# Optimization experiments

Measured on AMD Instinct MI355X. Metric: run time of the kernel, lower is better.

Reference implementation:

```python
import jax, jax.numpy as jnp
import numpy as np

B, T, D_MODEL = 1, 2048, 4096
NUM_Q_HEADS, NUM_KV_HEADS, KEY_SIZE = 32, 8, 128
ATTN_MULT = 0.08838834764831845  # 1/sqrt(key_size)
MAX_ATTN_VAL = 30.0


def rotate_half(x):
    x1, x2 = jnp.split(x, 2, axis=-1)
    return jnp.concatenate((-x2, x1), axis=-1)


def apply_rope(x):
    # x: [b, t, h, d]; offset = 0, positions = arange(t)
    b, t, h, d = x.shape
    exponents = jnp.arange(0, d, 2, dtype=jnp.float32)
    inv_freq = 1.0 / (10000.0 ** (exponents / d))            # [d/2]
    pos = jnp.arange(t, dtype=jnp.float32)                   # [t]
    phase = pos[:, None] * inv_freq[None, :]                 # [t, d/2]
    phase = jnp.tile(phase, (1, 2))[None, :, None, :]        # [1, t, 1, d] (tiled, not interleaved)
    return (x * jnp.cos(phase) + rotate_half(x) * jnp.sin(phase)).astype(x.dtype)


def setup_inputs() -> dict:
    key = jax.random.key(0)
    ks = jax.random.split(key, 8)
    query = jax.random.normal(ks[0], (B, T, D_MODEL), dtype=jnp.float32)
    kk = jax.random.normal(ks[1], (B, T, D_MODEL), dtype=jnp.float32)
    vv = jax.random.normal(ks[2], (B, T, D_MODEL), dtype=jnp.float32)
    mask = jnp.tril(jnp.ones((T, T), dtype=bool))[None, None, :, :]  # causal [1,1,T,T]
    s = 0.02
    Wq = jax.random.normal(ks[3], (D_MODEL, NUM_Q_HEADS * KEY_SIZE), dtype=jnp.float32) * s
    Wk = jax.random.normal(ks[4], (D_MODEL, NUM_KV_HEADS * KEY_SIZE), dtype=jnp.float32) * s
    Wv = jax.random.normal(ks[5], (D_MODEL, NUM_KV_HEADS * KEY_SIZE), dtype=jnp.float32) * s
    Wo = jax.random.normal(ks[6], (NUM_Q_HEADS * KEY_SIZE, D_MODEL), dtype=jnp.float32) * s
    return {"query": query, "key": kk, "value": vv, "mask": mask,
            "Wq": Wq, "Wk": Wk, "Wv": Wv, "Wo": Wo}


def reference(query, key, value, mask, Wq, Wk, Wv, Wo):
    b, t, _ = query.shape
    d = KEY_SIZE
    h, kv_h = NUM_Q_HEADS, NUM_KV_HEADS
    g = h // kv_h
    # projections (no bias)
    q = (query @ Wq).reshape(b, t, h, d)
    k = (key @ Wk).reshape(b, t, kv_h, d)
    v = (value @ Wv).reshape(b, t, kv_h, d)
    # RoPE on q and k
    q = apply_rope(q)
    k = apply_rope(k)
    # GQA grouping: [b, t, kv_h, g, d]
    q = q.reshape(b, t, kv_h, g, d)
    logits = jnp.einsum('btkgd,bTkd->bkgtT', q, k).astype(jnp.float32)
    logits = logits * ATTN_MULT
    logits = MAX_ATTN_VAL * jnp.tanh(logits / MAX_ATTN_VAL)  # soft-capping
    m = mask[:, :, None, :, :]  # [b,1,1,t,T]
    logits = jnp.where(m, logits, -1e30)
    weights = jax.nn.softmax(logits, axis=-1).astype(query.dtype)
    attn = jnp.einsum('bkgtT,bTkd->btkgd', weights, v)
    attn = attn.reshape(b, t, h * d)
    return attn @ Wo
```

## Files before the change

### kernel.cpp

```cpp
#include <hip/hip_runtime.h>
#include <hip/hip_bf16.h>
#include <stdint.h>
#include <stddef.h>

#define T_SEQ 2048
#define DM    4096
#define NQH   32
#define NKVH  8
#define HD    128
#define ATTN_MULT 0.08838834764831845f

typedef __attribute__((ext_vector_type(8))) short bf16x8;
typedef __attribute__((ext_vector_type(4))) float f32x4;
typedef __attribute__((ext_vector_type(4))) unsigned int u32x4;

__device__ __forceinline__ unsigned short f2b(float f) {
  unsigned u = __builtin_bit_cast(unsigned, f);
  u = u + 0x7FFFu + ((u >> 16) & 1u);
  return (unsigned short)(u >> 16);
}
__device__ __forceinline__ float b2f(unsigned short h) {
  unsigned u = ((unsigned)h) << 16;
  return __builtin_bit_cast(float, u);
}

typedef const __attribute__((address_space(1))) void* gptr1_t;
typedef __attribute__((address_space(3))) void* lptr3_t;
__device__ __forceinline__ void gl_lds16(const void* g, void* l) {
  __builtin_amdgcn_global_load_lds((gptr1_t)g, (lptr3_t)l, 16, 0, 0);
}

#define MFMA16(a, b, c) __builtin_amdgcn_mfma_f32_16x16x32_bf16((a), (b), (c), 0, 0, 0)

__global__ __launch_bounds__(256) void transpose_cast4_kernel(
    const float* __restrict__ Wq, const float* __restrict__ Wk,
    const float* __restrict__ Wv, const float* __restrict__ Wo,
    unsigned short* __restrict__ WqT, unsigned short* __restrict__ WkT,
    unsigned short* __restrict__ WvT, unsigned short* __restrict__ WoT) {
  __shared__ float tile[64][65];
  int y = blockIdx.y;
  const float* W;
  unsigned short* WT;
  int N, n0;
  if (y < 64)      { W = Wq; WT = WqT; N = 4096; n0 = y * 64; }
  else if (y < 80) { W = Wk; WT = WkT; N = 1024; n0 = (y - 64) * 64; }
  else if (y < 96) { W = Wv; WT = WvT; N = 1024; n0 = (y - 80) * 64; }
  else             { W = Wo; WT = WoT; N = 4096; n0 = (y - 96) * 64; }
  const int K = 4096;
  int k0 = blockIdx.x * 64;
  int t = threadIdx.x;
  int rr = t >> 4;
  int cc = t & 15;
#pragma unroll
  for (int c = 0; c < 4; ++c) {
    int row = c * 16 + rr;
    float4 v = *(const float4*)&W[(size_t)(k0 + row) * N + n0 + cc * 4];
    tile[row][cc * 4 + 0] = v.x;
    tile[row][cc * 4 + 1] = v.y;
    tile[row][cc * 4 + 2] = v.z;
    tile[row][cc * 4 + 3] = v.w;
  }
  __syncthreads();
  int orow = t >> 2;
  int kb = (t & 3) * 16;
  u32x4 o1, o2;
#pragma unroll
  for (int u = 0; u < 4; ++u) {
    o1[u] = (unsigned)f2b(tile[kb + 2 * u][orow]) |
            ((unsigned)f2b(tile[kb + 2 * u + 1][orow]) << 16);
    o2[u] = (unsigned)f2b(tile[kb + 8 + 2 * u][orow]) |
            ((unsigned)f2b(tile[kb + 9 + 2 * u][orow]) << 16);
  }
  unsigned short* dst = &WT[(size_t)(n0 + orow) * K + k0 + kb];
  *(u32x4*)dst = o1;
  *(u32x4*)(dst + 8) = o2;
}

__global__ __launch_bounds__(256) void cast3_kernel(
    const float* __restrict__ a0, const float* __restrict__ a1, const float* __restrict__ a2,
    unsigned short* __restrict__ b0, unsigned short* __restrict__ b1, unsigned short* __restrict__ b2) {
  const float* in = blockIdx.z == 0 ? a0 : (blockIdx.z == 1 ? a1 : a2);
  unsigned short* out = blockIdx.z == 0 ? b0 : (blockIdx.z == 1 ? b1 : b2);
  size_t idx = ((size_t)blockIdx.x * 256 + threadIdx.x) * 8;
  float4 x = *(const float4*)(in + idx);
  float4 y = *(const float4*)(in + idx + 4);
  u32x4 v;
  v[0] = (unsigned)f2b(x.x) | ((unsigned)f2b(x.y) << 16);
  v[1] = (unsigned)f2b(x.z) | ((unsigned)f2b(x.w) << 16);
  v[2] = (unsigned)f2b(y.x) | ((unsigned)f2b(y.y) << 16);
  v[3] = (unsigned)f2b(y.z) | ((unsigned)f2b(y.w) << 16);
  *(u32x4*)(out + idx) = v;
}

template <bool F32OUT>
__device__ __forceinline__ void gemm_dp_body(
    unsigned short* lds,
    const unsigned short* __restrict__ A, const unsigned short* __restrict__ BT,
    void* __restrict__ C, int N, int K, int m0, int n0) {
  int t = threadIdx.x;
  int w = t >> 6, l = t & 63;
  int wm = w >> 2, wn = w & 3;
  int lr = l & 15, lh = l >> 4;

  f32x4 acc[4][4] = {};

  int lrow8 = l >> 3;
  int scb = ((l & 7) ^ lrow8) << 4;
  const int NT = K >> 6;

  auto stage2 = [&](int tt, int bsel, int c0) {
    int kb = tt * 64;
#pragma unroll
    for (int c = 0; c < 2; ++c) {
      int chunk = w * 6 + c0 + c;
      if (chunk < 16) {
        const char* src = (const char*)A +
            ((size_t)(m0 + chunk * 8 + lrow8) * K + kb) * 2 + scb;
        gl_lds16(src, (char*)lds + bsel * 49152 + chunk * 1024);
      } else {
        const char* src = (const char*)BT +
            ((size_t)(n0 + (chunk - 16) * 8 + lrow8) * K + kb) * 2 + scb;
        gl_lds16(src, (char*)lds + bsel * 49152 + 16384 + (chunk - 16) * 1024);
      }
    }
  };

  stage2(0, 0, 0); stage2(0, 0, 2); stage2(0, 0, 4);
  stage2(1, 1, 0); stage2(1, 1, 2); stage2(1, 1, 4);
  asm volatile("s_waitcnt vmcnt(6)" ::: "memory");
  __builtin_amdgcn_s_barrier();

  int bsel = 0, bnext = 2;
  for (int tt = 0; tt < NT; ++tt) {
    bool pre = (tt + 2 < NT);
    const char* Ab = (const char*)lds + bsel * 49152;
    const char* Bb = Ab + 16384;
    int rswz = (lr & 7) << 4;
    int arow = wm * 64 + lr;
    int brow = wn * 64 + lr;
    int cb0 = (lh * 16) ^ rswz;
    int cb1 = (64 + lh * 16) ^ rswz;

    bf16x8 a0 = *(const bf16x8*)(Ab + (arow + 0) * 128 + cb0);
    bf16x8 a1 = *(const bf16x8*)(Ab + (arow + 16) * 128 + cb0);
    bf16x8 b0 = *(const bf16x8*)(Bb + (brow + 0) * 128 + cb0);
    bf16x8 b1 = *(const bf16x8*)(Bb + (brow + 16) * 128 + cb0);
    bf16x8 b2 = *(const bf16x8*)(Bb + (brow + 32) * 128 + cb0);
    bf16x8 b3 = *(const bf16x8*)(Bb + (brow + 48) * 128 + cb0);
    if (pre) stage2(tt + 2, bnext, 0);
    __builtin_amdgcn_s_barrier();
    __builtin_amdgcn_s_setprio(1);
    acc[0][0] = MFMA16(a0, b0, acc[0][0]);
    acc[0][1] = MFMA16(a0, b1, acc[0][1]);
    acc[0][2] = MFMA16(a0, b2, acc[0][2]);
    acc[0][3] = MFMA16(a0, b3, acc[0][3]);
    acc[1][0] = MFMA16(a1, b0, acc[1][0]);
    acc[1][1] = MFMA16(a1, b1, acc[1][1]);
    acc[1][2] = MFMA16(a1, b2, acc[1][2]);
    acc[1][3] = MFMA16(a1, b3, acc[1][3]);
    __builtin_amdgcn_s_setprio(0);
    __builtin_amdgcn_s_barrier();

    a0 = *(const bf16x8*)(Ab + (arow + 32) * 128 + cb0);
    a1 = *(const bf16x8*)(Ab + (arow + 48) * 128 + cb0);
    if (pre) stage2(tt + 2, bnext, 2);
    __builtin_amdgcn_s_barrier();
    __builtin_amdgcn_s_setprio(1);
    acc[2][0] = MFMA16(a0, b0, acc[2][0]);
    acc[2][1] = MFMA16(a0, b1, acc[2][1]);
    acc[2][2] = MFMA16(a0, b2, acc[2][2]);
    acc[2][3] = MFMA16(a0, b3, acc[2][3]);
    acc[3][0] = MFMA16(a1, b0, acc[3][0]);
    acc[3][1] = MFMA16(a1, b1, acc[3][1]);
    acc[3][2] = MFMA16(a1, b2, acc[3][2]);
    acc[3][3] = MFMA16(a1, b3, acc[3][3]);
    __builtin_amdgcn_s_setprio(0);
    __builtin_amdgcn_s_barrier();

    a0 = *(const bf16x8*)(Ab + (arow + 0) * 128 + cb1);
    a1 = *(const bf16x8*)(Ab + (arow + 16) * 128 + cb1);
    b0 = *(const bf16x8*)(Bb + (brow + 0) * 128 + cb1);
    b1 = *(const bf16x8*)(Bb + (brow + 16) * 128 + cb1);
    b2 = *(const bf16x8*)(Bb + (brow + 32) * 128 + cb1);
    b3 = *(const bf16x8*)(Bb + (brow + 48) * 128 + cb1);
    if (pre) stage2(tt + 2, bnext, 4);
    __builtin_amdgcn_s_barrier();
    __builtin_amdgcn_s_setprio(1);
    acc[0][0] = MFMA16(a0, b0, acc[0][0]);
    acc[0][1] = MFMA16(a0, b1, acc[0][1]);
    acc[0][2] = MFMA16(a0, b2, acc[0][2]);
    acc[0][3] = MFMA16(a0, b3, acc[0][3]);
    acc[1][0] = MFMA16(a1, b0, acc[1][0]);
    acc[1][1] = MFMA16(a1, b1, acc[1][1]);
    acc[1][2] = MFMA16(a1, b2, acc[1][2]);
    acc[1][3] = MFMA16(a1, b3, acc[1][3]);
    __builtin_amdgcn_s_setprio(0);
    __builtin_amdgcn_s_barrier();

    a0 = *(const bf16x8*)(Ab + (arow + 32) * 128 + cb1);
    a1 = *(const bf16x8*)(Ab + (arow + 48) * 128 + cb1);
    __builtin_amdgcn_s_barrier();
    __builtin_amdgcn_s_setprio(1);
    acc[2][0] = MFMA16(a0, b0, acc[2][0]);
    acc[2][1] = MFMA16(a0, b1, acc[2][1]);
    acc[2][2] = MFMA16(a0, b2, acc[2][2]);
    acc[2][3] = MFMA16(a0, b3, acc[2][3]);
    acc[3][0] = MFMA16(a1, b0, acc[3][0]);
    acc[3][1] = MFMA16(a1, b1, acc[3][1]);
    acc[3][2] = MFMA16(a1, b2, acc[3][2]);
    acc[3][3] = MFMA16(a1, b3, acc[3][3]);
    __builtin_amdgcn_s_setprio(0);
    if (pre) asm volatile("s_waitcnt vmcnt(6)" ::: "memory");
    else     asm volatile("s_waitcnt vmcnt(0)" ::: "memory");
    __builtin_amdgcn_s_barrier();
    bsel = (bsel == 2) ? 0 : bsel + 1;
    bnext = (bnext == 2) ? 0 : bnext + 1;
  }

#pragma unroll
  for (int i = 0; i < 4; ++i) {
#pragma unroll
    for (int j = 0; j < 4; ++j) {
#pragma unroll
      for (int r = 0; r < 4; ++r) {
        int row = m0 + wm * 64 + i * 16 + lh * 4 + r;
        int col = n0 + wn * 64 + j * 16 + lr;
        if constexpr (F32OUT)
          ((float*)C)[(size_t)row * N + col] = acc[i][j][r];
        else
          ((unsigned short*)C)[(size_t)row * N + col] = f2b(acc[i][j][r]);
      }
    }
  }
}

__global__ __launch_bounds__(512, 1) void qkv_dp_kernel(
    const unsigned short* __restrict__ qb, const unsigned short* __restrict__ WqT, unsigned short* __restrict__ Qp,
    const unsigned short* __restrict__ kb, const unsigned short* __restrict__ WkT, unsigned short* __restrict__ Kp,
    const unsigned short* __restrict__ vb, const unsigned short* __restrict__ WvT, unsigned short* __restrict__ Vp) {
  __shared__ unsigned short lds[3 * 24576];
  int flat = blockIdx.x;
  const unsigned short *A, *BT;
  unsigned short* C;
  int N, m0, n0;
  if (flat < 256) {
    A = qb; BT = WqT; C = Qp; N = NQH * HD;
    int xcd = flat & 7, idx = flat >> 3;
    n0 = (xcd * 2 + (idx & 1)) * 256;
    m0 = (idx >> 1) * 128;
  } else {
    int lf = flat - 256;
    int sel = lf >> 6;
    int local = lf & 63;
    A = sel ? vb : kb;
    BT = sel ? WvT : WkT;
    C = sel ? Vp : Kp;
    N = NKVH * HD;
    m0 = (local >> 2) * 128;
    n0 = (local & 3) * 256;
  }
  gemm_dp_body<false>(lds, A, BT, C, N, DM, m0, n0);
}

__global__ __launch_bounds__(512, 1) void gemm_dp_kernel(
    const unsigned short* __restrict__ A, const unsigned short* __restrict__ BT,
    float* __restrict__ C, int M, int N, int K) {
  __shared__ unsigned short lds[3 * 24576];
  int nx = gridDim.x;
  int flat = blockIdx.y * nx + blockIdx.x;
  int npx = nx >> 3;
  int xcd = flat & 7, idx = flat >> 3;
  int n0 = (xcd * npx + idx % npx) * 256;
  int m0 = (idx / npx) * 128;
  gemm_dp_body<true>(lds, A, BT, C, N, K, m0, n0);
}

__global__ __launch_bounds__(256) void sincos_kernel(float2* __restrict__ tab) {
  int idx = blockIdx.x * 256 + threadIdx.x;
  int i = idx & 63;
  int tpos = idx >> 6;
  float invf = exp2f(-(float)i * (13.287712379549449f / 64.0f));
  float phase = (float)tpos * invf;
  float s, c;
  sincosf(phase, &s, &c);
  tab[idx] = make_float2(c, s);
}

__global__ __launch_bounds__(256) void rope_kernel(unsigned short* __restrict__ X,
                                                   const float2* __restrict__ tab,
                                                   int hshift, float scale) {
  int idx = blockIdx.x * 256 + threadIdx.x;
  int i = idx & 63;
  int rest = idx >> 6;
  int nheads = 1 << hshift;
  int hh = rest & (nheads - 1);
  int tpos = rest >> hshift;
  float2 cs = tab[tpos * 64 + i];
  size_t base = (size_t)tpos * ((size_t)nheads * HD) + (size_t)hh * HD + i;
  float x1 = b2f(X[base]);
  float x2 = b2f(X[base + 64]);
  X[base] = f2b((x1 * cs.x - x2 * cs.y) * scale);
  X[base + 64] = f2b((x2 * cs.x + x1 * cs.y) * scale);
}

__global__ __launch_bounds__(256) void vtrans_kernel(
    const unsigned short* __restrict__ V, unsigned short* __restrict__ VT) {
  size_t flat = ((size_t)blockIdx.x * 256 + threadIdx.x) * 8;
  int t8 = (int)(flat & (T_SEQ - 1));
  int dh = (int)(flat >> 11);
  u32x4 v;
#pragma unroll
  for (int u = 0; u < 4; ++u) {
    unsigned short lo = V[(size_t)(t8 + 2 * u) * (NKVH * HD) + dh];
    unsigned short hi = V[(size_t)(t8 + 2 * u + 1) * (NKVH * HD) + dh];
    v[u] = (unsigned)lo | ((unsigned)hi << 16);
  }
  *(u32x4*)(VT + flat) = v;
}

template <bool DIAG>
__device__ __forceinline__ void softmax_frag(const f32x4 s[4], float& lsum, bf16x8 pf[2],
                                             int lr, int lh, int wq) {
  constexpr float C2f = (float)(-60.0 * 1.4426950408889634);
  float pv[4][4];
#pragma unroll
  for (int ct = 0; ct < 4; ++ct)
#pragma unroll
    for (int r = 0; r < 4; ++r) {
      float u = exp2f(s[ct][r]);
      float p = exp2f(C2f * __builtin_amdgcn_rcpf(u + 1.0f));
      if constexpr (DIAG) {
        int kg = ct * 16 + lh * 4 + r;
        int qg = wq * 16 + lr;
        if (kg > qg) p = 0.0f;
      }
      pv[ct][r] = p;
      lsum += p;
    }
  unsigned pk[4][2];
#pragma unroll
  for (int ct = 0; ct < 4; ++ct) {
    pk[ct][0] = (unsigned)f2b(pv[ct][0]) | ((unsigned)f2b(pv[ct][1]) << 16);
    pk[ct][1] = (unsigned)f2b(pv[ct][2]) | ((unsigned)f2b(pv[ct][3]) << 16);
  }
  int s0 = ((lh & 1) << 5) + lr;
  int s1 = s0 + 16;
  bool hi = (lh >= 2);
#pragma unroll
  for (int ks = 0; ks < 2; ++ks) {
    unsigned a0 = (unsigned)__shfl((int)pk[2 * ks][0], s0, 64);
    unsigned a1 = (unsigned)__shfl((int)pk[2 * ks][1], s0, 64);
    unsigned a2 = (unsigned)__shfl((int)pk[2 * ks][0], s1, 64);
    unsigned a3 = (unsigned)__shfl((int)pk[2 * ks][1], s1, 64);
    unsigned b0 = (unsigned)__shfl((int)pk[2 * ks + 1][0], s0, 64);
    unsigned b1 = (unsigned)__shfl((int)pk[2 * ks + 1][1], s0, 64);
    unsigned b2 = (unsigned)__shfl((int)pk[2 * ks + 1][0], s1, 64);
    unsigned b3 = (unsigned)__shfl((int)pk[2 * ks + 1][1], s1, 64);
    u32x4 f;
    f[0] = hi ? b0 : a0;
    f[1] = hi ? b1 : a1;
    f[2] = hi ? b2 : a2;
    f[3] = hi ? b3 : a3;
    pf[ks] = __builtin_bit_cast(bf16x8, f);
  }
}

template <bool WITHA, bool DIAGA, bool DIAGB>
__device__ __forceinline__ void attn_tile(
    const char* KsCur, const char* VsCur,
    const bf16x8 qfA[4], const bf16x8 qfB[4],
    f32x4 oaccA[8], f32x4 oaccB[8],
    float& lsumA, float& lsumB,
    int lr, int lh, int wq) {
  f32x4 sB[4], sA[4];
#pragma unroll
  for (int ct = 0; ct < 4; ++ct) {
    f32x4 zB = {};
    f32x4 zA = {};
#pragma unroll
    for (int kk = 0; kk < 4; ++kk) {
      int row = ct * 16 + lr;
      int cb = (kk * 32 + lh * 8) * 2;
      bf16x8 kf = *(const bf16x8*)(KsCur + row * 256 + (cb ^ ((row & 7) << 4)));
      zB = MFMA16(kf, qfB[kk], zB);
      if constexpr (WITHA) zA = MFMA16(kf, qfA[kk], zA);
    }
    sB[ct] = zB;
    if constexpr (WITHA) sA[ct] = zA;
  }
  bf16x8 pfB[2], pfA[2];
  softmax_frag<DIAGB>(sB, lsumB, pfB, lr, lh, wq);
  if constexpr (WITHA) softmax_frag<DIAGA>(sA, lsumA, pfA, lr, lh, wq);
#pragma unroll
  for (int ks = 0; ks < 2; ++ks) {
    int pcb = (ks * 32 + lh * 8) * 2;
#pragma unroll
    for (int dt = 0; dt < 8; ++dt) {
      int vrow = dt * 16 + lr;
      bf16x8 vf = *(const bf16x8*)(VsCur + ((vrow * 128 + pcb) ^ ((vrow & 7) << 4)));
      oaccB[dt] = MFMA16(pfB[ks], vf, oaccB[dt]);
      if constexpr (WITHA) oaccA[dt] = MFMA16(pfA[ks], vf, oaccA[dt]);
    }
  }
}

__global__ __launch_bounds__(512, 2) void attn_kernel(
    const unsigned short* __restrict__ Q,
    const unsigned short* __restrict__ Kx,
    const unsigned short* __restrict__ VT,
    unsigned short* __restrict__ O) {
  __shared__ unsigned short Ks[2][64 * 128];
  __shared__ unsigned short Vs[2][128 * 64];

  int bx = blockIdx.x;
  int by = blockIdx.y;
  int qtA = bx, qtB = 31 - bx;
  int t = threadIdx.x;
  int w = t >> 6, l = t & 63;
  int wq = w & 3;
  int hh = by * 2 + (w >> 2);
  int kvh = by >> 1;
  int lr = l & 15, lh = l >> 4;

  bf16x8 qfA[4], qfB[4];
  {
    const unsigned short* qpA = Q + (size_t)(qtA * 64 + wq * 16 + lr) * (NQH * HD) + hh * HD + lh * 8;
    const unsigned short* qpB = Q + (size_t)(qtB * 64 + wq * 16 + lr) * (NQH * HD) + hh * HD + lh * 8;
#pragma unroll
    for (int kk = 0; kk < 4; ++kk) {
      qfA[kk] = *(const bf16x8*)(qpA + kk * 32);
      qfB[kk] = *(const bf16x8*)(qpB + kk * 32);
    }
  }

  f32x4 oaccA[8] = {}, oaccB[8] = {};
  float lsumA = 0.f, lsumB = 0.f;

  const char* KgB = (const char*)Kx + (size_t)kvh * HD * 2;
  const char* VgB = (const char*)VT + (size_t)kvh * HD * T_SEQ * 2;

  auto stage = [&](int kt, int b) {
#pragma unroll
    for (int c = 0; c < 2; ++c) {
      int chunk = w * 2 + c;
      int p = chunk * 1024 + l * 16;
      {
        int row = p >> 8;
        int cb = p & 255;
        int cbl = cb ^ ((row & 7) << 4);
        gl_lds16(KgB + (size_t)(kt * 64 + row) * (NKVH * HD * 2) + cbl,
                 (char*)Ks[b] + chunk * 1024);
      }
      {
        int row = p >> 7;
        int cb = p & 127;
        int cbl = cb ^ ((row & 7) << 4);
        gl_lds16(VgB + (size_t)row * (T_SEQ * 2) + (size_t)kt * 128 + cbl,
                 (char*)Vs[b] + chunk * 1024);
      }
    }
  };

  stage(0, 0);
  __syncthreads();

  int cur = 0;
  for (int kt = 0; kt <= qtB; ++kt) {
    if (kt < qtB) stage(kt + 1, cur ^ 1);
    const char* Kc = (const char*)Ks[cur];
    const char* Vc = (const char*)Vs[cur];
    if (kt < qtA)
      attn_tile<true, false, false>(Kc, Vc, qfA, qfB, oaccA, oaccB, lsumA, lsumB, lr, lh, wq);
    else if (kt == qtA)
      attn_tile<true, true, false>(Kc, Vc, qfA, qfB, oaccA, oaccB, lsumA, lsumB, lr, lh, wq);
    else if (kt < qtB)
      attn_tile<false, false, false>(Kc, Vc, qfA, qfB, oaccA, oaccB, lsumA, lsumB, lr, lh, wq);
    else
      attn_tile<false, false, true>(Kc, Vc, qfA, qfB, oaccA, oaccB, lsumA, lsumB, lr, lh, wq);
    __syncthreads();
    cur ^= 1;
  }

  lsumB += __shfl_xor(lsumB, 16, 64);
  lsumB += __shfl_xor(lsumB, 32, 64);
  lsumA += __shfl_xor(lsumA, 16, 64);
  lsumA += __shfl_xor(lsumA, 32, 64);

#pragma unroll
  for (int i = 0; i < 4; ++i) {
    int srcl = (l & 48) | (lh * 4 + i);
    float invB = 1.0f / __shfl(lsumB, srcl, 64);
    float invA = 1.0f / __shfl(lsumA, srcl, 64);
    int qgB = qtB * 64 + wq * 16 + lh * 4 + i;
    int qgA = qtA * 64 + wq * 16 + lh * 4 + i;
#pragma unroll
    for (int dt = 0; dt < 8; ++dt) {
      O[(size_t)qgB * (NQH * HD) + hh * HD + dt * 16 + lr] = f2b(oaccB[dt][i] * invB);
      O[(size_t)qgA * (NQH * HD) + hh * HD + dt * 16 + lr] = f2b(oaccA[dt][i] * invA);
    }
  }
}

extern "C" void kernel_launch(void* const* d_in, const int* in_sizes, int n_in,
                              void* d_out, int out_size, void* d_ws, size_t ws_size,
                              hipStream_t stream) {
  const float* query = (const float*)d_in[0];
  const float* key = (const float*)d_in[1];
  const float* value = (const float*)d_in[2];
  const float* Wq = (const float*)d_in[4];
  const float* Wk = (const float*)d_in[5];
  const float* Wv = (const float*)d_in[6];
  const float* Wo = (const float*)d_in[7];
  float* out = (float*)d_out;

  char* ws = (char*)d_ws;
  constexpr size_t OFF_WQT = 0;
  constexpr size_t OFF_WOT = 33554432;
  constexpr size_t OFF_WKT = 67108864;
  constexpr size_t OFF_WVT = 75497472;
  constexpr size_t OFF_QB = 83886080;
  constexpr size_t OFF_KB = 100663296;
  constexpr size_t OFF_VB = 117440512;
  constexpr size_t OFF_QP = 134217728;
  constexpr size_t OFF_KP = 150994944;
  constexpr size_t OFF_VP = 155189248;
  constexpr size_t OFF_VT = 159383552;
  constexpr size_t OFF_AT = 163577856;
  constexpr size_t WS_NEED = 180355072;
  if (ws_size < WS_NEED) return;

  unsigned short* WqT = (unsigned short*)(ws + OFF_WQT);
  unsigned short* WoT = (unsigned short*)(ws + OFF_WOT);
  unsigned short* WkT = (unsigned short*)(ws + OFF_WKT);
  unsigned short* WvT = (unsigned short*)(ws + OFF_WVT);
  unsigned short* qb = (unsigned short*)(ws + OFF_QB);
  unsigned short* kb = (unsigned short*)(ws + OFF_KB);
  unsigned short* vb = (unsigned short*)(ws + OFF_VB);
  unsigned short* Qp = (unsigned short*)(ws + OFF_QP);
  unsigned short* Kp = (unsigned short*)(ws + OFF_KP);
  unsigned short* Vp = (unsigned short*)(ws + OFF_VP);
  unsigned short* VTb = (unsigned short*)(ws + OFF_VT);
  unsigned short* attnb = (unsigned short*)(ws + OFF_AT);
  float2* tab = (float2*)(ws + OFF_QB);

  transpose_cast4_kernel<<<dim3(64, 160), 256, 0, stream>>>(
      Wq, Wk, Wv, Wo, WqT, WkT, WvT, WoT);
  cast3_kernel<<<dim3(4096, 1, 3), 256, 0, stream>>>(query, key, value, qb, kb, vb);
  qkv_dp_kernel<<<dim3(384), 512, 0, stream>>>(qb, WqT, Qp, kb, WkT, Kp, vb, WvT, Vp);
  sincos_kernel<<<dim3(T_SEQ * 64 / 256), 256, 0, stream>>>(tab);
  constexpr float C1 = (float)(0.08838834764831845 * 1.4426950408889634 / 15.0);
  rope_kernel<<<dim3(T_SEQ * NQH * 64 / 256), 256, 0, stream>>>(Qp, tab, 5, C1);
  rope_kernel<<<dim3(T_SEQ * NKVH * 64 / 256), 256, 0, stream>>>(Kp, tab, 3, 1.0f);
  vtrans_kernel<<<dim3(NKVH * HD * T_SEQ / (256 * 8)), 256, 0, stream>>>(Vp, VTb);
  attn_kernel<<<dim3(16, 16), 512, 0, stream>>>(Qp, Kp, VTb, attnb);
  gemm_dp_kernel<<<dim3(16, 16), 512, 0, stream>>>(attnb, WoT, out, T_SEQ, DM, DM);
}
```

Before: 407.2 us.

## Use 256x256 GEMM tiles with double buffering and split-K output projection

Replaces the 128x256 triple-buffered GEMM body with a 256x256 tile that uses double-buffered LDS, so each block reuses more data per loaded tile and moves less global memory per FLOP. The QKV projection now launches half as many blocks. The output projection uses split-K over two K halves, writing two fp32 partial buffers that a separate kernel adds together, so the grid still fills the device. The trade-offs are more accumulator registers, a shallower prefetch pipeline with full vmcnt(0) waits, and extra fp32 traffic plus a launch for the reduction.

```diff
diff --git a/kernel.cpp b/kernel.cpp
--- a/kernel.cpp
+++ b/kernel.cpp
@@ -93,137 +93,135 @@
 }
 
 template <bool F32OUT>
-__device__ __forceinline__ void gemm_dp_body(
+__device__ __forceinline__ void gemm256_body(
     unsigned short* lds,
     const unsigned short* __restrict__ A, const unsigned short* __restrict__ BT,
-    void* __restrict__ C, int N, int K, int m0, int n0) {
+    void* __restrict__ C, int N, int Klen, int Kstride, int m0, int n0) {
   int t = threadIdx.x;
   int w = t >> 6, l = t & 63;
   int wm = w >> 2, wn = w & 3;
   int lr = l & 15, lh = l >> 4;
 
-  f32x4 acc[4][4] = {};
-
-  int lrow8 = l >> 3;
-  int scb = ((l & 7) ^ lrow8) << 4;
-  const int NT = K >> 6;
-
-  auto stage2 = [&](int tt, int bsel, int c0) {
-    int kb = tt * 64;
-#pragma unroll
-    for (int c = 0; c < 2; ++c) {
-      int chunk = w * 6 + c0 + c;
-      if (chunk < 16) {
-        const char* src = (const char*)A +
-            ((size_t)(m0 + chunk * 8 + lrow8) * K + kb) * 2 + scb;
-        gl_lds16(src, (char*)lds + bsel * 49152 + chunk * 1024);
-      } else {
-        const char* src = (const char*)BT +
-            ((size_t)(n0 + (chunk - 16) * 8 + lrow8) * K + kb) * 2 + scb;
-        gl_lds16(src, (char*)lds + bsel * 49152 + 16384 + (chunk - 16) * 1024);
-      }
+  f32x4 acc[8][4] = {};
+
+  int scb = (((l & 7) ^ (l >> 3)) & 7) << 4;
+  const int NT = Klen >> 6;
+  int rswz = (lr & 7) << 4;
+  int cb0 = (lh * 16) ^ rswz;
+  int cb1 = (64 + lh * 16) ^ rswz;
+
+  auto stageT = [&](const unsigned short* X, int base, int tt, int c, int ldsoff) {
+#pragma unroll
+    for (int h = 0; h < 2; ++h) {
+      int grow = base + h * 128 + w * 8 + (l >> 3);
+      const char* s1 = (const char*)X + ((size_t)grow * Kstride + tt * 64) * 2 + scb;
+      gl_lds16(s1, (char*)lds + c * 65536 + ldsoff + h * 16384 + w * 1024);
+      const char* s2 = (const char*)X + ((size_t)(grow + 64) * Kstride + tt * 64) * 2 + scb;
+      gl_lds16(s2, (char*)lds + c * 65536 + ldsoff + h * 16384 + 8192 + w * 1024);
     }
   };
 
-  stage2(0, 0, 0); stage2(0, 0, 2); stage2(0, 0, 4);
-  stage2(1, 1, 0); stage2(1, 1, 2); stage2(1, 1, 4);
-  asm volatile("s_waitcnt vmcnt(6)" ::: "memory");
+  stageT(A, m0, 0, 0, 0);
+  stageT(BT, n0, 0, 0, 32768);
+  asm volatile("s_waitcnt vmcnt(0)" ::: "memory");
   __builtin_amdgcn_s_barrier();
 
-  int bsel = 0, bnext = 2;
   for (int tt = 0; tt < NT; ++tt) {
-    bool pre = (tt + 2 < NT);
-    const char* Ab = (const char*)lds + bsel * 49152;
-    const char* Bb = Ab + 16384;
-    int rswz = (lr & 7) << 4;
-    int arow = wm * 64 + lr;
+    const char* Ab = (const char*)lds + (tt & 1) * 65536;
+    const char* Bb = Ab + 32768;
+    bool pre = (tt + 1 < NT);
+    int nb = (tt + 1) & 1;
+    int arow = wm * 128 + lr;
     int brow = wn * 64 + lr;
-    int cb0 = (lh * 16) ^ rswz;
-    int cb1 = (64 + lh * 16) ^ rswz;
-
-    bf16x8 a0 = *(const bf16x8*)(Ab + (arow + 0) * 128 + cb0);
-    bf16x8 a1 = *(const bf16x8*)(Ab + (arow + 16) * 128 + cb0);
-    bf16x8 b0 = *(const bf16x8*)(Bb + (brow + 0) * 128 + cb0);
-    bf16x8 b1 = *(const bf16x8*)(Bb + (brow + 16) * 128 + cb0);
-    bf16x8 b2 = *(const bf16x8*)(Bb + (brow + 32) * 128 + cb0);
-    bf16x8 b3 = *(const bf16x8*)(Bb + (brow + 48) * 128 + cb0);
-    if (pre) stage2(tt + 2, bnext, 0);
+    bf16x8 a0, a1, a2, a3, b0, b1, b2, b3;
+
+    a0 = *(const bf16x8*)(Ab + (arow + 0) * 128 + cb0);
+    a1 = *(const bf16x8*)(Ab + (arow + 16) * 128 + cb0);
+    a2 = *(const bf16x8*)(Ab + (arow + 32) * 128 + cb0);
+    a3 = *(const bf16x8*)(Ab + (arow + 48) * 128 + cb0);
+    b0 = *(const bf16x8*)(Bb + (brow + 0) * 128 + cb0);
+    b1 = *(const bf16x8*)(Bb + (brow + 16) * 128 + cb0);
+    b2 = *(const bf16x8*)(Bb + (brow + 32) * 128 + cb0);
+    b3 = *(const bf16x8*)(Bb + (brow + 48) * 128 + cb0);
+    if (pre) stageT(A, m0, tt + 1, nb, 0);
     __builtin_amdgcn_s_barrier();
     __builtin_amdgcn_s_setprio(1);
-    acc[0][0] = MFMA16(a0, b0, acc[0][0]);
-    acc[0][1] = MFMA16(a0, b1, acc[0][1]);
-    acc[0][2] = MFMA16(a0, b2, acc[0][2]);
-    acc[0][3] = MFMA16(a0, b3, acc[0][3]);
-    acc[1][0] = MFMA16(a1, b0, acc[1][0]);
-    acc[1][1] = MFMA16(a1, b1, acc[1][1]);
-    acc[1][2] = MFMA16(a1, b2, acc[1][2]);
-    acc[1][3] = MFMA16(a1, b3, acc[1][3]);
+    acc[0][0] = MFMA16(a0, b0, acc[0][0]); acc[0][1] = MFMA16(a0, b1, acc[0][1]);
+    acc[0][2] = MFMA16(a0, b2, acc[0][2]); acc[0][3] = MFMA16(a0, b3, acc[0][3]);
+    acc[1][0] = MFMA16(a1, b0, acc[1][0]); acc[1][1] = MFMA16(a1, b1, acc[1][1]);
+    acc[1][2] = MFMA16(a1, b2, acc[1][2]); acc[1][3] = MFMA16(a1, b3, acc[1][3]);
+    acc[2][0] = MFMA16(a2, b0, acc[2][0]); acc[2][1] = MFMA16(a2, b1, acc[2][1]);
+    acc[2][2] = MFMA16(a2, b2, acc[2][2]); acc[2][3] = MFMA16(a2, b3, acc[2][3]);
+    acc[3][0] = MFMA16(a3, b0, acc[3][0]); acc[3][1] = MFMA16(a3, b1, acc[3][1]);
+    acc[3][2] = MFMA16(a3, b2, acc[3][2]); acc[3][3] = MFMA16(a3, b3, acc[3][3]);
     __builtin_amdgcn_s_setprio(0);
     __builtin_amdgcn_s_barrier();
 
-    a0 = *(const bf16x8*)(Ab + (arow + 32) * 128 + cb0);
-    a1 = *(const bf16x8*)(Ab + (arow + 48) * 128 + cb0);
-    if (pre) stage2(tt + 2, bnext, 2);
+    a0 = *(const bf16x8*)(Ab + (arow + 64) * 128 + cb0);
+    a1 = *(const bf16x8*)(Ab + (arow + 80) * 128 + cb0);
+    a2 = *(const bf16x8*)(Ab + (arow + 96) * 128 + cb0);
+    a3 = *(const bf16x8*)(Ab + (arow + 112) * 128 + cb0);
+    if (pre) stageT(BT, n0, tt + 1, nb, 32768);
     __builtin_amdgcn_s_barrier();
     __builtin_amdgcn_s_setprio(1);
-    acc[2][0] = MFMA16(a0, b0, acc[2][0]);
-    acc[2][1] = MFMA16(a0, b1, acc[2][1]);
-    acc[2][2] = MFMA16(a0, b2, acc[2][2]);
-    acc[2][3] = MFMA16(a0, b3, acc[2][3]);
-    acc[3][0] = MFMA16(a1, b0, acc[3][0]);
-    acc[3][1] = MFMA16(a1, b1, acc[3][1]);
-    acc[3][2] = MFMA16(a1, b2, acc[3][2]);
-    acc[3][3] = MFMA16(a1, b3, acc[3][3]);
+    acc[4][0] = MFMA16(a0, b0, acc[4][0]); acc[4][1] = MFMA16(a0, b1, acc[4][1]);
+    acc[4][2] = MFMA16(a0, b2, acc[4][2]); acc[4][3] = MFMA16(a0, b3, acc[4][3]);
+    acc[5][0] = MFMA16(a1, b0, acc[5][0]); acc[5][1] = MFMA16(a1, b1, acc[5][1]);
+    acc[5][2] = MFMA16(a1, b2, acc[5][2]); acc[5][3] = MFMA16(a1, b3, acc[5][3]);
+    acc[6][0] = MFMA16(a2, b0, acc[6][0]); acc[6][1] = MFMA16(a2, b1, acc[6][1]);
+    acc[6][2] = MFMA16(a2, b2, acc[6][2]); acc[6][3] = MFMA16(a2, b3, acc[6][3]);
+    acc[7][0] = MFMA16(a3, b0, acc[7][0]); acc[7][1] = MFMA16(a3, b1, acc[7][1]);
+    acc[7][2] = MFMA16(a3, b2, acc[7][2]); acc[7][3] = MFMA16(a3, b3, acc[7][3]);
     __builtin_amdgcn_s_setprio(0);
     __builtin_amdgcn_s_barrier();
 
     a0 = *(const bf16x8*)(Ab + (arow + 0) * 128 + cb1);
     a1 = *(const bf16x8*)(Ab + (arow + 16) * 128 + cb1);
+    a2 = *(const bf16x8*)(Ab + (arow + 32) * 128 + cb1);
+    a3 = *(const bf16x8*)(Ab + (arow + 48) * 128 + cb1);
     b0 = *(const bf16x8*)(Bb + (brow + 0) * 128 + cb1);
     b1 = *(const bf16x8*)(Bb + (brow + 16) * 128 + cb1);
     b2 = *(const bf16x8*)(Bb + (brow + 32) * 128 + cb1);
     b3 = *(const bf16x8*)(Bb + (brow + 48) * 128 + cb1);
-    if (pre) stage2(tt + 2, bnext, 4);
     __builtin_amdgcn_s_barrier();
     __builtin_amdgcn_s_setprio(1);
-    acc[0][0] = MFMA16(a0, b0, acc[0][0]);
-    acc[0][1] = MFMA16(a0, b1, acc[0][1]);
-    acc[0][2] = MFMA16(a0, b2, acc[0][2]);
-    acc[0][3] = MFMA16(a0, b3, acc[0][3]);
-    acc[1][0] = MFMA16(a1, b0, acc[1][0]);
-    acc[1][1] = MFMA16(a1, b1, acc[1][1]);
-    acc[1][2] = MFMA16(a1, b2, acc[1][2]);
-    acc[1][3] = MFMA16(a1, b3, acc[1][3]);
+    acc[0][0] = MFMA16(a0, b0, acc[0][0]); acc[0][1] = MFMA16(a0, b1, acc[0][1]);
+    acc[0][2] = MFMA16(a0, b2, acc[0][2]); acc[0][3] = MFMA16(a0, b3, acc[0][3]);
+    acc[1][0] = MFMA16(a1, b0, acc[1][0]); acc[1][1] = MFMA16(a1, b1, acc[1][1]);
+    acc[1][2] = MFMA16(a1, b2, acc[1][2]); acc[1][3] = MFMA16(a1, b3, acc[1][3]);
+    acc[2][0] = MFMA16(a2, b0, acc[2][0]); acc[2][1] = MFMA16(a2, b1, acc[2][1]);
+    acc[2][2] = MFMA16(a2, b2, acc[2][2]); acc[2][3] = MFMA16(a2, b3, acc[2][3]);
+    acc[3][0] = MFMA16(a3, b0, acc[3][0]); acc[3][1] = MFMA16(a3, b1, acc[3][1]);
+    acc[3][2] = MFMA16(a3, b2, acc[3][2]); acc[3][3] = MFMA16(a3, b3, acc[3][3]);
     __builtin_amdgcn_s_setprio(0);
     __builtin_amdgcn_s_barrier();
 
-    a0 = *(const bf16x8*)(Ab + (arow + 32) * 128 + cb1);
-    a1 = *(const bf16x8*)(Ab + (arow + 48) * 128 + cb1);
+    a0 = *(const bf16x8*)(Ab + (arow + 64) * 128 + cb1);
+    a1 = *(const bf16x8*)(Ab + (arow + 80) * 128 + cb1);
+    a2 = *(const bf16x8*)(Ab + (arow + 96) * 128 + cb1);
+    a3 = *(const bf16x8*)(Ab + (arow + 112) * 128 + cb1);
     __builtin_amdgcn_s_barrier();
     __builtin_amdgcn_s_setprio(1);
-    acc[2][0] = MFMA16(a0, b0, acc[2][0]);
-    acc[2][1] = MFMA16(a0, b1, acc[2][1]);
-    acc[2][2] = MFMA16(a0, b2, acc[2][2]);
-    acc[2][3] = MFMA16(a0, b3, acc[2][3]);
-    acc[3][0] = MFMA16(a1, b0, acc[3][0]);
-    acc[3][1] = MFMA16(a1, b1, acc[3][1]);
-    acc[3][2] = MFMA16(a1, b2, acc[3][2]);
-    acc[3][3] = MFMA16(a1, b3, acc[3][3]);
+    acc[4][0] = MFMA16(a0, b0, acc[4][0]); acc[4][1] = MFMA16(a0, b1, acc[4][1]);
+    acc[4][2] = MFMA16(a0, b2, acc[4][2]); acc[4][3] = MFMA16(a0, b3, acc[4][3]);
+    acc[5][0] = MFMA16(a1, b0, acc[5][0]); acc[5][1] = MFMA16(a1, b1, acc[5][1]);
+    acc[5][2] = MFMA16(a1, b2, acc[5][2]); acc[5][3] = MFMA16(a1, b3, acc[5][3]);
+    acc[6][0] = MFMA16(a2, b0, acc[6][0]); acc[6][1] = MFMA16(a2, b1, acc[6][1]);
+    acc[6][2] = MFMA16(a2, b2, acc[6][2]); acc[6][3] = MFMA16(a2, b3, acc[6][3]);
+    acc[7][0] = MFMA16(a3, b0, acc[7][0]); acc[7][1] = MFMA16(a3, b1, acc[7][1]);
+    acc[7][2] = MFMA16(a3, b2, acc[7][2]); acc[7][3] = MFMA16(a3, b3, acc[7][3]);
     __builtin_amdgcn_s_setprio(0);
-    if (pre) asm volatile("s_waitcnt vmcnt(6)" ::: "memory");
-    else     asm volatile("s_waitcnt vmcnt(0)" ::: "memory");
-    __builtin_amdgcn_s_barrier();
-    bsel = (bsel == 2) ? 0 : bsel + 1;
-    bnext = (bnext == 2) ? 0 : bnext + 1;
-  }
-
-#pragma unroll
-  for (int i = 0; i < 4; ++i) {
+    asm volatile("s_waitcnt vmcnt(0)" ::: "memory");
+    __builtin_amdgcn_s_barrier();
+  }
+
+#pragma unroll
+  for (int i = 0; i < 8; ++i) {
 #pragma unroll
     for (int j = 0; j < 4; ++j) {
 #pragma unroll
       for (int r = 0; r < 4; ++r) {
-        int row = m0 + wm * 64 + i * 16 + lh * 4 + r;
+        int row = m0 + wm * 128 + i * 16 + lh * 4 + r;
         int col = n0 + wn * 64 + j * 16 + lr;
         if constexpr (F32OUT)
           ((float*)C)[(size_t)row * N + col] = acc[i][j][r];
@@ -234,45 +232,54 @@
   }
 }
 
-__global__ __launch_bounds__(512, 1) void qkv_dp_kernel(
+__global__ __launch_bounds__(512, 1) void qkv256_kernel(
     const unsigned short* __restrict__ qb, const unsigned short* __restrict__ WqT, unsigned short* __restrict__ Qp,
     const unsigned short* __restrict__ kb, const unsigned short* __restrict__ WkT, unsigned short* __restrict__ Kp,
     const unsigned short* __restrict__ vb, const unsigned short* __restrict__ WvT, unsigned short* __restrict__ Vp) {
-  __shared__ unsigned short lds[3 * 24576];
+  __shared__ unsigned short lds[2 * 32768];
   int flat = blockIdx.x;
   const unsigned short *A, *BT;
   unsigned short* C;
   int N, m0, n0;
-  if (flat < 256) {
+  if (flat < 128) {
     A = qb; BT = WqT; C = Qp; N = NQH * HD;
-    int xcd = flat & 7, idx = flat >> 3;
-    n0 = (xcd * 2 + (idx & 1)) * 256;
-    m0 = (idx >> 1) * 128;
+    m0 = (flat >> 4) * 256;
+    n0 = (flat & 15) * 256;
   } else {
-    int lf = flat - 256;
-    int sel = lf >> 6;
-    int local = lf & 63;
+    int lf = flat - 128;
+    int sel = lf >> 5;
+    int local = lf & 31;
     A = sel ? vb : kb;
     BT = sel ? WvT : WkT;
     C = sel ? Vp : Kp;
     N = NKVH * HD;
-    m0 = (local >> 2) * 128;
+    m0 = (local >> 2) * 256;
     n0 = (local & 3) * 256;
   }
-  gemm_dp_body<false>(lds, A, BT, C, N, DM, m0, n0);
-}
-
-__global__ __launch_bounds__(512, 1) void gemm_dp_kernel(
+  gemm256_body<false>(lds, A, BT, C, N, DM, DM, m0, n0);
+}
+
+__global__ __launch_bounds__(512, 1) void oproj256_kernel(
     const unsigned short* __restrict__ A, const unsigned short* __restrict__ BT,
-    float* __restrict__ C, int M, int N, int K) {
-  __shared__ unsigned short lds[3 * 24576];
-  int nx = gridDim.x;
-  int flat = blockIdx.y * nx + blockIdx.x;
-  int npx = nx >> 3;
-  int xcd = flat & 7, idx = flat >> 3;
-  int n0 = (xcd * npx + idx % npx) * 256;
-  int m0 = (idx / npx) * 128;
-  gemm_dp_body<true>(lds, A, BT, C, N, K, m0, n0);
+    float* __restrict__ P0, float* __restrict__ P1) {
+  __shared__ unsigned short lds[2 * 32768];
+  int flat = blockIdx.x;
+  int ksl = flat >> 7;
+  int local = flat & 127;
+  int m0 = (local >> 4) * 256;
+  int n0 = (local & 15) * 256;
+  gemm256_body<true>(lds, A + ksl * 2048, BT + ksl * 2048,
+                     ksl ? P1 : P0, DM, 2048, DM, m0, n0);
+}
+
+__global__ __launch_bounds__(256) void reduce_add_kernel(
+    const float* __restrict__ P0, const float* __restrict__ P1, float* __restrict__ out) {
+  size_t idx = ((size_t)blockIdx.x * 256 + threadIdx.x) * 4;
+  float4 a = *(const float4*)(P0 + idx);
+  float4 b = *(const float4*)(P1 + idx);
+  float4 r;
+  r.x = a.x + b.x; r.y = a.y + b.y; r.z = a.z + b.z; r.w = a.w + b.w;
+  *(float4*)(out + idx) = r;
 }
 
 __global__ __launch_bounds__(256) void sincos_kernel(float2* __restrict__ tab) {
@@ -542,16 +549,19 @@
   unsigned short* VTb = (unsigned short*)(ws + OFF_VT);
   unsigned short* attnb = (unsigned short*)(ws + OFF_AT);
   float2* tab = (float2*)(ws + OFF_QB);
+  float* P0 = (float*)(ws + OFF_QB);
+  float* P1 = (float*)(ws + OFF_VB);
 
   transpose_cast4_kernel<<<dim3(64, 160), 256, 0, stream>>>(
       Wq, Wk, Wv, Wo, WqT, WkT, WvT, WoT);
   cast3_kernel<<<dim3(4096, 1, 3), 256, 0, stream>>>(query, key, value, qb, kb, vb);
-  qkv_dp_kernel<<<dim3(384), 512, 0, stream>>>(qb, WqT, Qp, kb, WkT, Kp, vb, WvT, Vp);
+  qkv256_kernel<<<dim3(192), 512, 0, stream>>>(qb, WqT, Qp, kb, WkT, Kp, vb, WvT, Vp);
   sincos_kernel<<<dim3(T_SEQ * 64 / 256), 256, 0, stream>>>(tab);
   constexpr float C1 = (float)(0.08838834764831845 * 1.4426950408889634 / 15.0);
   rope_kernel<<<dim3(T_SEQ * NQH * 64 / 256), 256, 0, stream>>>(Qp, tab, 5, C1);
   rope_kernel<<<dim3(T_SEQ * NKVH * 64 / 256), 256, 0, stream>>>(Kp, tab, 3, 1.0f);
   vtrans_kernel<<<dim3(NKVH * HD * T_SEQ / (256 * 8)), 256, 0, stream>>>(Vp, VTb);
   attn_kernel<<<dim3(16, 16), 512, 0, stream>>>(Qp, Kp, VTb, attnb);
-  gemm_dp_kernel<<<dim3(16, 16), 512, 0, stream>>>(attnb, WoT, out, T_SEQ, DM, DM);
-}
+  oproj256_kernel<<<dim3(256), 512, 0, stream>>>(attnb, WoT, P0, P1);
+  reduce_add_kernel<<<dim3(T_SEQ * DM / (256 * 4)), 256, 0, stream>>>(P0, P1, out);
+}
```

After: 381.6 us. 6.3% less time.
